# Optimization experiments

Hardware: AMD Instinct MI355X
Metric: run time of the kernel (lower is better)

The kernel has to match this reference:

```python
import jax, jax.numpy as jnp
import numpy as np

N_NODES = 50000
N_EDGES = 800000
IN_FEATS = 256
OUT_FEATS = 128
NEG_SLOPE = 0.2


def setup_inputs() -> dict:
    key = jax.random.key(0)
    k1, k2, k3, k4 = jax.random.split(key, 4)
    feat = jax.random.normal(k1, (N_NODES, IN_FEATS), dtype=jnp.float32)
    limit = float(np.sqrt(6.0 / (IN_FEATS + OUT_FEATS)))  # xavier_uniform
    W = jax.random.uniform(k2, (IN_FEATS, OUT_FEATS), dtype=jnp.float32,
                           minval=-limit, maxval=limit)
    bias = jnp.zeros((OUT_FEATS,), dtype=jnp.float32)
    src = jax.random.randint(k3, (N_EDGES,), 0, N_NODES, dtype=jnp.int64)
    dst = jax.random.randint(k4, (N_EDGES,), 0, N_NODES, dtype=jnp.int64)
    return {"feat": feat, "W": W, "bias": bias, "src": src, "dst": dst}


def reference(feat, W, bias, src, dst):
    N = feat.shape[0]
    ones = jnp.ones(src.shape[0], dtype=feat.dtype)
    # degrees (clamped to 1, as in the torch code)
    out_deg = jnp.maximum(jax.ops.segment_sum(ones, src, num_segments=N), 1.0)
    in_deg = jnp.maximum(jax.ops.segment_sum(ones, dst, num_segments=N), 1.0)
    # norm == 'both': pre-scale by out-degree^-1/2
    h = feat * (out_deg ** -0.5)[:, None]
    # in_feats > out_feats branch: project first
    h = h @ W  # [N, out_feats]
    hs = h[src]          # [E, out_feats] gather
    hd = jnp.tanh(h[dst])  # [E, out_feats] gather
    e = jnp.sum(hs * hd, axis=1)                      # [E]
    e = jnp.where(e > 0, e, NEG_SLOPE * e)            # leaky_relu(0.2)
    # edge_softmax: softmax over edges grouped by destination node
    emax = jax.ops.segment_max(e, dst, num_segments=N)
    emax = jnp.where(jnp.isfinite(emax), emax, 0.0)   # guard empty groups
    ee = jnp.exp(e - emax[dst])
    esum = jax.ops.segment_sum(ee, dst, num_segments=N)
    e_soft = ee / esum[dst]
    # update_all(copy_u, sum): unweighted scatter-sum of src features into dst
    rst = jax.ops.segment_sum(hs, dst, num_segments=N)  # [N, out_feats]
    # norm == 'both': post-scale by in-degree^-1/2, then bias (activation=None)
    rst = rst * (in_deg ** -0.5)[:, None] + bias
    return rst, e_soft
```

## Files before the change

### kernel.cpp

```cpp
#include <hip/hip_runtime.h>
#include <math.h>

#define NNODES 50000
#define NEDGES 800000
#define INFEAT 256
#define OUTF   128
#define NEG_SLOPE 0.2f
#define MAXDEG 64
#define GBM 64
#define GEMM_NB 782

typedef __attribute__((ext_vector_type(8))) short bf16x8;
typedef __attribute__((ext_vector_type(4))) float f32x4;

__device__ __forceinline__ ushort f2bf(float f) {
    unsigned u = __float_as_uint(f);
    unsigned r = (u + 0x7FFFu + ((u >> 16) & 1u)) >> 16;
    return (ushort)r;
}
__device__ __forceinline__ float bflo(unsigned u) { return __uint_as_float(u << 16); }
__device__ __forceinline__ float bfhi(unsigned u) { return __uint_as_float(u & 0xFFFF0000u); }

__global__ void kzero(int* p, int n) {
    int i = blockIdx.x * 256 + threadIdx.x;
    if (i < n) p[i] = 0;
}

__global__ void kwbt(const float* __restrict__ W, ushort* __restrict__ whi,
                     ushort* __restrict__ wlo) {
    int i = blockIdx.x * 256 + threadIdx.x;
    int n = i >> 8, k = i & 255;
    float w = W[(size_t)k * OUTF + n];
    ushort h = f2bf(w);
    float hf = __uint_as_float((unsigned)h << 16);
    whi[i] = h;
    wlo[i] = f2bf(w - hf);
}

__launch_bounds__(256)
__global__ void kfused(const float* __restrict__ feat, const uint4* __restrict__ whi,
                       const uint4* __restrict__ wlo, unsigned* __restrict__ hb,
                       const int* __restrict__ src, const int* __restrict__ dst,
                       int* __restrict__ cnt_out, int* __restrict__ fill,
                       int* __restrict__ ebd, int M, int E) {
    __shared__ char smem_raw[32768];
    int tid = threadIdx.x;

    if (blockIdx.x & 1) {
        for (int i = (blockIdx.x >> 1) * 256 + tid; i < E; i += GEMM_NB * 256) {
            atomicAdd(&cnt_out[src[i]], 1);
            int d = dst[i];
            int p = atomicAdd(&fill[d], 1);
            if (p < MAXDEG) ebd[(d << 6) + p] = i;
        }
        return;
    }

    uint4* Bh = (uint4*)smem_raw;
    uint4* Bo = Bh + 1024;
    int lane = tid & 63, wid = tid >> 6;
    int gb = blockIdx.x >> 1;

    int m0 = gb * GBM + wid * 16;
    int arow = m0 + (lane & 15);
    int ar = arow < M ? arow : M - 1;
    const float* ap = &feat[(size_t)ar * INFEAT + ((lane >> 4) << 3)];

    union { uint4 u; bf16x8 s; } ahi[8], alo[8];
    #pragma unroll
    for (int ks = 0; ks < 8; ks++) {
        float4 a0 = *(const float4*)&ap[ks * 32];
        float4 a1 = *(const float4*)&ap[ks * 32 + 4];
        float av[8] = {a0.x, a0.y, a0.z, a0.w, a1.x, a1.y, a1.z, a1.w};
        unsigned hw[4], lw[4];
        #pragma unroll
        for (int q = 0; q < 4; q++) {
            asm("v_cvt_pk_bf16_f32 %0, %1, %2" : "=v"(hw[q]) : "v"(av[2*q]), "v"(av[2*q+1]));
            float h0 = bflo(hw[q]);
            float h1 = bfhi(hw[q]);
            float l0 = av[2*q] - h0;
            float l1 = av[2*q+1] - h1;
            asm("v_cvt_pk_bf16_f32 %0, %1, %2" : "=v"(lw[q]) : "v"(l0), "v"(l1));
        }
        ahi[ks].u = make_uint4(hw[0], hw[1], hw[2], hw[3]);
        alo[ks].u = make_uint4(lw[0], lw[1], lw[2], lw[3]);
    }

    f32x4 acc[8];
    #pragma unroll
    for (int i = 0; i < 8; i++) acc[i] = (f32x4){0.f, 0.f, 0.f, 0.f};

    #pragma unroll
    for (int h = 0; h < 4; h++) {
        __syncthreads();
        #pragma unroll
        for (int r = 0; r < 4; r++) {
            int g = tid + 256 * r;
            int nl = g >> 5, kc = g & 31;
            int gi = (h * 32 + nl) * 32 + kc;
            int li = (nl << 5) | (kc ^ (nl & 7));
            Bh[li] = whi[gi];
            Bo[li] = wlo[gi];
        }
        __syncthreads();
        #pragma unroll
        for (int ks = 0; ks < 8; ks++) {
            int kcb = (ks << 2) + (lane >> 4);
            #pragma unroll
            for (int nt = 0; nt < 2; nt++) {
                int nl = (nt << 4) | (lane & 15);
                int li = (nl << 5) | (kcb ^ (nl & 7));
                union { uint4 u; bf16x8 s; } bh, bo;
                bh.u = Bh[li];
                bo.u = Bo[li];
                int ai = h * 2 + nt;
                acc[ai] = __builtin_amdgcn_mfma_f32_16x16x32_bf16(ahi[ks].s, bh.s, acc[ai], 0, 0, 0);
                acc[ai] = __builtin_amdgcn_mfma_f32_16x16x32_bf16(alo[ks].s, bh.s, acc[ai], 0, 0, 0);
                acc[ai] = __builtin_amdgcn_mfma_f32_16x16x32_bf16(ahi[ks].s, bo.s, acc[ai], 0, 0, 0);
            }
        }
    }

    #pragma unroll
    for (int ai = 0; ai < 8; ai++) {
        #pragma unroll
        for (int q = 0; q < 4; q++) {
            float v = acc[ai][q];
            float vp = __shfl_xor(v, 1, 64);
            int grow = m0 + ((lane >> 4) << 2) + q;
            if (!(lane & 1) && grow < M) {
                unsigned w;
                asm("v_cvt_pk_bf16_f32 %0, %1, %2" : "=v"(w) : "v"(v), "v"(vp));
                hb[(size_t)grow * 64 + ((ai << 4) | (lane & 15)) / 2] = w;
            }
        }
    }
}

__launch_bounds__(256)
__global__ void kaggregate(const unsigned* __restrict__ hb, const int* __restrict__ src,
                           const int* __restrict__ ebd, const int* __restrict__ fill,
                           const int* __restrict__ cnt_out, const float* __restrict__ bias,
                           float* __restrict__ out_rst, float* __restrict__ out_es,
                           int nnodes) {
    __shared__ float thl[4][128];
    int wid = threadIdx.x >> 6;
    int lane = threadIdx.x & 63;
    int n = blockIdx.x * 4 + wid;
    if (n >= nnodes) return;

    int deg = fill[n];
    if (deg > MAXDEG) deg = MAXDEG;
    const int ROWU = OUTF / 2;

    int g = lane >> 3;
    int t = lane & 7;
    int c = t * 16;

    {
        int co = cnt_out[n];
        float sc_d = rsqrtf((float)(co < 1 ? 1 : co));
        unsigned u = hb[(size_t)n * ROWU + lane];
        thl[wid][2 * lane]     = tanhf(sc_d * bflo(u));
        thl[wid][2 * lane + 1] = tanhf(sc_d * bfhi(u));
    }
    float thf[16];
    #pragma unroll
    for (int q = 0; q < 4; q++) {
        float4 v = *(float4*)&thl[wid][c + q * 4];
        thf[q*4+0] = v.x; thf[q*4+1] = v.y; thf[q*4+2] = v.z; thf[q*4+3] = v.w;
    }

    int eid = 0, s = 0;
    if (lane < deg) { eid = ebd[(n << 6) + lane]; s = src[eid]; }

    float accf[16];
    #pragma unroll
    for (int k = 0; k < 16; k++) accf[k] = 0.f;
    float myv = -INFINITY;

    for (int base = 0; base < deg; base += 8) {
        int m = base + g;
        int sj = __shfl(s, m, 64);
        uint4 r0 = make_uint4(0u, 0u, 0u, 0u), r1 = r0;
        float scs = 0.f;
        if (m < deg) {
            const uint4* rp = (const uint4*)&hb[(size_t)sj * ROWU + t * 8];
            r0 = rp[0]; r1 = rp[1];
            int co = cnt_out[sj];
            scs = rsqrtf((float)(co < 1 ? 1 : co));
        }
        unsigned ua[8] = {r0.x, r0.y, r0.z, r0.w, r1.x, r1.y, r1.z, r1.w};
        float pd = 0.f;
        #pragma unroll
        for (int k = 0; k < 8; k++) {
            float lo = bflo(ua[k]), hi = bfhi(ua[k]);
            accf[2*k]   = fmaf(scs, lo, accf[2*k]);
            accf[2*k+1] = fmaf(scs, hi, accf[2*k+1]);
            pd += lo * thf[2*k] + hi * thf[2*k+1];
        }
        #pragma unroll
        for (int msk = 1; msk < 8; msk <<= 1) pd += __shfl_xor(pd, msk, 64);
        float p = scs * pd;
        float e = p > 0.f ? p : NEG_SLOPE * p;
        if (m < deg && t == (base >> 3)) myv = e;
    }

    if (deg > 0) {
        float mx = myv;
        #pragma unroll
        for (int msk = 1; msk < 64; msk <<= 1) mx = fmaxf(mx, __shfl_xor(mx, msk, 64));
        int m = 8 * t + g;
        float v = (m < deg) ? expf(myv - mx) : 0.f;
        float sum = v;
        #pragma unroll
        for (int msk = 1; msk < 64; msk <<= 1) sum += __shfl_xor(sum, msk, 64);
        float inv = 1.f / sum;
        int eidm = __shfl(eid, m, 64);
        if (m < deg) out_es[eidm] = v * inv;
    }

    #pragma unroll
    for (int msk = 8; msk < 64; msk <<= 1) {
        #pragma unroll
        for (int k = 0; k < 16; k++) accf[k] += __shfl_xor(accf[k], msk, 64);
    }
    if (g == 0) {
        float sc = rsqrtf((float)(deg < 1 ? 1 : deg));
        #pragma unroll
        for (int q = 0; q < 4; q++) {
            float4 b = *(const float4*)&bias[c + q * 4];
            float4 r = make_float4(accf[4*q]   * sc + b.x, accf[4*q+1] * sc + b.y,
                                   accf[4*q+2] * sc + b.z, accf[4*q+3] * sc + b.w);
            *(float4*)&out_rst[(size_t)n * OUTF + c + q * 4] = r;
        }
    }
}

extern "C" void kernel_launch(void* const* d_in, const int* in_sizes, int n_in,
                              void* d_out, int out_size, void* d_ws, size_t ws_size,
                              hipStream_t stream) {
    const float* feat = (const float*)d_in[0];
    const float* W    = (const float*)d_in[1];
    const float* bias = (const float*)d_in[2];
    const int*   src  = (const int*)d_in[3];
    const int*   dst  = (const int*)d_in[4];

    float* out_rst = (float*)d_out;
    float* out_es  = (float*)d_out + (size_t)NNODES * OUTF;

    char* ws = (char*)d_ws;
    size_t o = 0;
    auto alloc = [&](size_t bytes) { void* p = ws + o; o += (bytes + 255) & ~(size_t)255; return p; };
    int*    cnt_out = (int*)alloc(NNODES * 4);
    int*    fill    = (int*)alloc(NNODES * 4);
    int*    ebd     = (int*)alloc((size_t)NNODES * MAXDEG * 4);
    ushort* whi     = (ushort*)alloc((size_t)OUTF * INFEAT * 2);
    ushort* wlo     = (ushort*)alloc((size_t)OUTF * INFEAT * 2);
    ushort* hb      = (ushort*)alloc((size_t)NNODES * OUTF * 2);
    (void)o; (void)ws_size; (void)in_sizes; (void)n_in; (void)out_size;

    const int zints = (int)(2 * (((size_t)NNODES * 4 + 255) & ~(size_t)255) / 4);
    kzero<<<(zints + 255) / 256, 256, 0, stream>>>((int*)d_ws, zints);

    kwbt<<<(OUTF * INFEAT + 255) / 256, 256, 0, stream>>>(W, whi, wlo);

    kfused<<<2 * GEMM_NB, 256, 0, stream>>>(feat, (const uint4*)whi, (const uint4*)wlo,
                                            (unsigned*)hb, src, dst,
                                            cnt_out, fill, ebd, NNODES, NEDGES);

    kaggregate<<<(NNODES + 3) / 4, 256, 0, stream>>>((const unsigned*)hb, src, ebd, fill,
                                                     cnt_out, bias, out_rst, out_es, NNODES);
}
```

Measured before the change: 137.6 us.

## Split CSR bucketing across kernels to overlap with aggregation of first node range

Bucketing by destination is now done in two parts. Nodes below a split point are bucketed in the fused GEMM kernel, and the rest are bucketed in a new mixed kernel whose other blocks already aggregate the first node range. A final kernel then aggregates the remaining nodes. The aim is to shorten the atomic-heavy bucketing that sits alongside the GEMM and to overlap the rest with aggregation work, at the cost of an extra launch and reading dst twice. The zeroing kernel is also replaced with hipMemsetAsync.

Result: slower. 144.1 us (+4.7%).

```diff
diff --git a/kernel.cpp b/kernel.cpp
--- a/kernel.cpp
+++ b/kernel.cpp
@@ -9,6 +9,8 @@
 #define MAXDEG 64
 #define GBM 64
 #define GEMM_NB 782
+#define HSPLIT 20000
+#define AGG1_NB 5000
 
 typedef __attribute__((ext_vector_type(8))) short bf16x8;
 typedef __attribute__((ext_vector_type(4))) float f32x4;
@@ -20,11 +22,6 @@
 }
 __device__ __forceinline__ float bflo(unsigned u) { return __uint_as_float(u << 16); }
 __device__ __forceinline__ float bfhi(unsigned u) { return __uint_as_float(u & 0xFFFF0000u); }
-
-__global__ void kzero(int* p, int n) {
-    int i = blockIdx.x * 256 + threadIdx.x;
-    if (i < n) p[i] = 0;
-}
 
 __global__ void kwbt(const float* __restrict__ W, ushort* __restrict__ whi,
                      ushort* __restrict__ wlo) {
@@ -37,6 +34,104 @@
     wlo[i] = f2bf(w - hf);
 }
 
+__device__ __forceinline__ void agg_node(int n, float* thlw,
+                                         const unsigned* __restrict__ hb,
+                                         const int* __restrict__ src,
+                                         const int* __restrict__ ebd,
+                                         const int* __restrict__ fill,
+                                         const int* __restrict__ cnt_out,
+                                         const float* __restrict__ bias,
+                                         float* __restrict__ out_rst,
+                                         float* __restrict__ out_es) {
+    int lane = threadIdx.x & 63;
+    int deg = fill[n];
+    if (deg > MAXDEG) deg = MAXDEG;
+    const int ROWU = OUTF / 2;
+
+    int g = lane >> 3;
+    int t = lane & 7;
+    int c = t * 16;
+
+    {
+        int co = cnt_out[n];
+        float sc_d = rsqrtf((float)(co < 1 ? 1 : co));
+        unsigned u = hb[(size_t)n * ROWU + lane];
+        thlw[2 * lane]     = tanhf(sc_d * bflo(u));
+        thlw[2 * lane + 1] = tanhf(sc_d * bfhi(u));
+    }
+    float thf[16];
+    #pragma unroll
+    for (int q = 0; q < 4; q++) {
+        float4 v = *(float4*)&thlw[c + q * 4];
+        thf[q*4+0] = v.x; thf[q*4+1] = v.y; thf[q*4+2] = v.z; thf[q*4+3] = v.w;
+    }
+
+    int eid = 0, s = 0;
+    if (lane < deg) { eid = ebd[(n << 6) + lane]; s = src[eid]; }
+
+    float accf[16];
+    #pragma unroll
+    for (int k = 0; k < 16; k++) accf[k] = 0.f;
+    float myv = -INFINITY;
+
+    for (int base = 0; base < deg; base += 8) {
+        int m = base + g;
+        int sj = __shfl(s, m, 64);
+        uint4 r0 = make_uint4(0u, 0u, 0u, 0u), r1 = r0;
+        float scs = 0.f;
+        if (m < deg) {
+            const uint4* rp = (const uint4*)&hb[(size_t)sj * ROWU + t * 8];
+            r0 = rp[0]; r1 = rp[1];
+            int co = cnt_out[sj];
+            scs = rsqrtf((float)(co < 1 ? 1 : co));
+        }
+        unsigned ua[8] = {r0.x, r0.y, r0.z, r0.w, r1.x, r1.y, r1.z, r1.w};
+        float pd = 0.f;
+        #pragma unroll
+        for (int k = 0; k < 8; k++) {
+            float lo = bflo(ua[k]), hi = bfhi(ua[k]);
+            accf[2*k]   = fmaf(scs, lo, accf[2*k]);
+            accf[2*k+1] = fmaf(scs, hi, accf[2*k+1]);
+            pd += lo * thf[2*k] + hi * thf[2*k+1];
+        }
+        #pragma unroll
+        for (int msk = 1; msk < 8; msk <<= 1) pd += __shfl_xor(pd, msk, 64);
+        float p = scs * pd;
+        float e = p > 0.f ? p : NEG_SLOPE * p;
+        if (m < deg && t == (base >> 3)) myv = e;
+    }
+
+    if (deg > 0) {
+        float mx = myv;
+        #pragma unroll
+        for (int msk = 1; msk < 64; msk <<= 1) mx = fmaxf(mx, __shfl_xor(mx, msk, 64));
+        int m = 8 * t + g;
+        float v = (m < deg) ? expf(myv - mx) : 0.f;
+        float sum = v;
+        #pragma unroll
+        for (int msk = 1; msk < 64; msk <<= 1) sum += __shfl_xor(sum, msk, 64);
+        float inv = 1.f / sum;
+        int eidm = __shfl(eid, m, 64);
+        if (m < deg) out_es[eidm] = v * inv;
+    }
+
+    #pragma unroll
+    for (int msk = 8; msk < 64; msk <<= 1) {
+        #pragma unroll
+        for (int k = 0; k < 16; k++) accf[k] += __shfl_xor(accf[k], msk, 64);
+    }
+    if (g == 0) {
+        float sc = rsqrtf((float)(deg < 1 ? 1 : deg));
+        #pragma unroll
+        for (int q = 0; q < 4; q++) {
+            float4 b = *(const float4*)&bias[c + q * 4];
+            float4 r = make_float4(accf[4*q]   * sc + b.x, accf[4*q+1] * sc + b.y,
+                                   accf[4*q+2] * sc + b.z, accf[4*q+3] * sc + b.w);
+            *(float4*)&out_rst[(size_t)n * OUTF + c + q * 4] = r;
+        }
+    }
+}
+
 __launch_bounds__(256)
 __global__ void kfused(const float* __restrict__ feat, const uint4* __restrict__ whi,
                        const uint4* __restrict__ wlo, unsigned* __restrict__ hb,
@@ -50,8 +145,10 @@
         for (int i = (blockIdx.x >> 1) * 256 + tid; i < E; i += GEMM_NB * 256) {
             atomicAdd(&cnt_out[src[i]], 1);
             int d = dst[i];
-            int p = atomicAdd(&fill[d], 1);
-            if (p < MAXDEG) ebd[(d << 6) + p] = i;
+            if (d < HSPLIT) {
+                int p = atomicAdd(&fill[d], 1);
+                if (p < MAXDEG) ebd[(d << 6) + p] = i;
+            }
         }
         return;
     }
@@ -138,103 +235,42 @@
 }
 
 __launch_bounds__(256)
-__global__ void kaggregate(const unsigned* __restrict__ hb, const int* __restrict__ src,
-                           const int* __restrict__ ebd, const int* __restrict__ fill,
-                           const int* __restrict__ cnt_out, const float* __restrict__ bias,
-                           float* __restrict__ out_rst, float* __restrict__ out_es,
-                           int nnodes) {
+__global__ void kmix(const unsigned* __restrict__ hb, const int* __restrict__ src,
+                     const int* __restrict__ dst, int* __restrict__ ebd,
+                     int* __restrict__ fill, const int* __restrict__ cnt_out,
+                     const float* __restrict__ bias, float* __restrict__ out_rst,
+                     float* __restrict__ out_es, int E) {
+    __shared__ float thl[4][128];
+    int tid = threadIdx.x;
+
+    if (blockIdx.x & 1) {
+        for (int i = (blockIdx.x >> 1) * 256 + tid; i < E; i += AGG1_NB * 256) {
+            int d = dst[i];
+            if (d >= HSPLIT) {
+                int p = atomicAdd(&fill[d], 1);
+                if (p < MAXDEG) ebd[(d << 6) + p] = i;
+            }
+        }
+        return;
+    }
+
+    int wid = tid >> 6;
+    int n = (blockIdx.x >> 1) * 4 + wid;
+    if (n >= HSPLIT) return;
+    agg_node(n, &thl[wid][0], hb, src, ebd, fill, cnt_out, bias, out_rst, out_es);
+}
+
+__launch_bounds__(256)
+__global__ void kagg(const unsigned* __restrict__ hb, const int* __restrict__ src,
+                     const int* __restrict__ ebd, const int* __restrict__ fill,
+                     const int* __restrict__ cnt_out, const float* __restrict__ bias,
+                     float* __restrict__ out_rst, float* __restrict__ out_es,
+                     int n0, int n1) {
     __shared__ float thl[4][128];
     int wid = threadIdx.x >> 6;
-    int lane = threadIdx.x & 63;
-    int n = blockIdx.x * 4 + wid;
-    if (n >= nnodes) return;
-
-    int deg = fill[n];
-    if (deg > MAXDEG) deg = MAXDEG;
-    const int ROWU = OUTF / 2;
-
-    int g = lane >> 3;
-    int t = lane & 7;
-    int c = t * 16;
-
-    {
-        int co = cnt_out[n];
-        float sc_d = rsqrtf((float)(co < 1 ? 1 : co));
-        unsigned u = hb[(size_t)n * ROWU + lane];
-        thl[wid][2 * lane]     = tanhf(sc_d * bflo(u));
-        thl[wid][2 * lane + 1] = tanhf(sc_d * bfhi(u));
-    }
-    float thf[16];
-    #pragma unroll
-    for (int q = 0; q < 4; q++) {
-        float4 v = *(float4*)&thl[wid][c + q * 4];
-        thf[q*4+0] = v.x; thf[q*4+1] = v.y; thf[q*4+2] = v.z; thf[q*4+3] = v.w;
-    }
-
-    int eid = 0, s = 0;
-    if (lane < deg) { eid = ebd[(n << 6) + lane]; s = src[eid]; }
-
-    float accf[16];
-    #pragma unroll
-    for (int k = 0; k < 16; k++) accf[k] = 0.f;
-    float myv = -INFINITY;
-
-    for (int base = 0; base < deg; base += 8) {
-        int m = base + g;
-        int sj = __shfl(s, m, 64);
-        uint4 r0 = make_uint4(0u, 0u, 0u, 0u), r1 = r0;
-        float scs = 0.f;
-        if (m < deg) {
-            const uint4* rp = (const uint4*)&hb[(size_t)sj * ROWU + t * 8];
-            r0 = rp[0]; r1 = rp[1];
-            int co = cnt_out[sj];
-            scs = rsqrtf((float)(co < 1 ? 1 : co));
-        }
-        unsigned ua[8] = {r0.x, r0.y, r0.z, r0.w, r1.x, r1.y, r1.z, r1.w};
-        float pd = 0.f;
-        #pragma unroll
-        for (int k = 0; k < 8; k++) {
-            float lo = bflo(ua[k]), hi = bfhi(ua[k]);
-            accf[2*k]   = fmaf(scs, lo, accf[2*k]);
-            accf[2*k+1] = fmaf(scs, hi, accf[2*k+1]);
-            pd += lo * thf[2*k] + hi * thf[2*k+1];
-        }
-        #pragma unroll
-        for (int msk = 1; msk < 8; msk <<= 1) pd += __shfl_xor(pd, msk, 64);
-        float p = scs * pd;
-        float e = p > 0.f ? p : NEG_SLOPE * p;
-        if (m < deg && t == (base >> 3)) myv = e;
-    }
-
-    if (deg > 0) {
-        float mx = myv;
-        #pragma unroll
-        for (int msk = 1; msk < 64; msk <<= 1) mx = fmaxf(mx, __shfl_xor(mx, msk, 64));
-        int m = 8 * t + g;
-        float v = (m < deg) ? expf(myv - mx) : 0.f;
-        float sum = v;
-        #pragma unroll
-        for (int msk = 1; msk < 64; msk <<= 1) sum += __shfl_xor(sum, msk, 64);
-        float inv = 1.f / sum;
-        int eidm = __shfl(eid, m, 64);
-        if (m < deg) out_es[eidm] = v * inv;
-    }
-
-    #pragma unroll
-    for (int msk = 8; msk < 64; msk <<= 1) {
-        #pragma unroll
-        for (int k = 0; k < 16; k++) accf[k] += __shfl_xor(accf[k], msk, 64);
-    }
-    if (g == 0) {
-        float sc = rsqrtf((float)(deg < 1 ? 1 : deg));
-        #pragma unroll
-        for (int q = 0; q < 4; q++) {
-            float4 b = *(const float4*)&bias[c + q * 4];
-            float4 r = make_float4(accf[4*q]   * sc + b.x, accf[4*q+1] * sc + b.y,
-                                   accf[4*q+2] * sc + b.z, accf[4*q+3] * sc + b.w);
-            *(float4*)&out_rst[(size_t)n * OUTF + c + q * 4] = r;
-        }
-    }
+    int n = n0 + blockIdx.x * 4 + wid;
+    if (n >= n1) return;
+    agg_node(n, &thl[wid][0], hb, src, ebd, fill, cnt_out, bias, out_rst, out_es);
 }
 
 extern "C" void kernel_launch(void* const* d_in, const int* in_sizes, int n_in,
@@ -260,8 +296,8 @@
     ushort* hb      = (ushort*)alloc((size_t)NNODES * OUTF * 2);
     (void)o; (void)ws_size; (void)in_sizes; (void)n_in; (void)out_size;
 
-    const int zints = (int)(2 * (((size_t)NNODES * 4 + 255) & ~(size_t)255) / 4);
-    kzero<<<(zints + 255) / 256, 256, 0, stream>>>((int*)d_ws, zints);
+    const size_t zbytes = 2 * (((size_t)NNODES * 4 + 255) & ~(size_t)255);
+    hipMemsetAsync(d_ws, 0, zbytes, stream);
 
     kwbt<<<(OUTF * INFEAT + 255) / 256, 256, 0, stream>>>(W, whi, wlo);
 
@@ -269,6 +305,10 @@
                                             (unsigned*)hb, src, dst,
                                             cnt_out, fill, ebd, NNODES, NEDGES);
 
-    kaggregate<<<(NNODES + 3) / 4, 256, 0, stream>>>((const unsigned*)hb, src, ebd, fill,
-                                                     cnt_out, bias, out_rst, out_es, NNODES);
-}
+    kmix<<<2 * AGG1_NB, 256, 0, stream>>>((const unsigned*)hb, src, dst, ebd, fill,
+                                          cnt_out, bias, out_rst, out_es, NEDGES);
+
+    kagg<<<(NNODES - HSPLIT + 3) / 4, 256, 0, stream>>>((const unsigned*)hb, src, ebd, fill,
+                                                        cnt_out, bias, out_rst, out_es,
+                                                        HSPLIT, NNODES);
+}
```

## Replace global out-degree atomics with per-block packed LDS histograms and reduction

Applied to the files above, without the earlier changes.

Out-degree counting moves from global atomicAdd per edge to 128 dedicated blocks that each build a shared-memory histogram, packing four 8-bit counters per word, then write partial histograms that a new reduction kernel sums into cnt_out. The zeroing kernel is replaced by a memset of only the fill array, and the aggregation body is factored into a device helper. This is meant to cut global atomic traffic and contention on cnt_out, at the cost of an extra kernel launch, about 6.4 MB of partial-histogram writes and reads, and 8-bit per-block counters that could overflow if one block saw more than 255 edges from the same source.

After: 117.8 us. -14.4%, faster.

```diff
diff --git a/kernel.cpp b/kernel.cpp
--- a/kernel.cpp
+++ b/kernel.cpp
@@ -9,6 +9,8 @@
 #define MAXDEG 64
 #define GBM 64
 #define GEMM_NB 782
+#define HB 128
+#define HW 12500
 
 typedef __attribute__((ext_vector_type(8))) short bf16x8;
 typedef __attribute__((ext_vector_type(4))) float f32x4;
@@ -20,11 +22,6 @@
 }
 __device__ __forceinline__ float bflo(unsigned u) { return __uint_as_float(u << 16); }
 __device__ __forceinline__ float bfhi(unsigned u) { return __uint_as_float(u & 0xFFFF0000u); }
-
-__global__ void kzero(int* p, int n) {
-    int i = blockIdx.x * 256 + threadIdx.x;
-    if (i < n) p[i] = 0;
-}
 
 __global__ void kwbt(const float* __restrict__ W, ushort* __restrict__ whi,
                      ushort* __restrict__ wlo) {
@@ -41,14 +38,27 @@
 __global__ void kfused(const float* __restrict__ feat, const uint4* __restrict__ whi,
                        const uint4* __restrict__ wlo, unsigned* __restrict__ hb,
                        const int* __restrict__ src, const int* __restrict__ dst,
-                       int* __restrict__ cnt_out, int* __restrict__ fill,
-                       int* __restrict__ ebd, int M, int E) {
-    __shared__ char smem_raw[32768];
+                       int* __restrict__ fill, int* __restrict__ ebd,
+                       unsigned* __restrict__ hist_part, int M, int E) {
+    __shared__ unsigned sh[HW + 300];
     int tid = threadIdx.x;
 
-    if (blockIdx.x & 1) {
-        for (int i = (blockIdx.x >> 1) * 256 + tid; i < E; i += GEMM_NB * 256) {
-            atomicAdd(&cnt_out[src[i]], 1);
+    if (blockIdx.x < HB) {
+        for (int j = tid; j < HW; j += 256) sh[j] = 0;
+        __syncthreads();
+        for (int i = blockIdx.x * 256 + tid; i < E; i += HB * 256) {
+            int s = src[i];
+            atomicAdd(&sh[s >> 2], 1u << ((s & 3) * 8));
+        }
+        __syncthreads();
+        unsigned* gp = hist_part + (size_t)blockIdx.x * HW;
+        for (int j = tid; j < HW; j += 256) gp[j] = sh[j];
+        return;
+    }
+
+    int b2 = blockIdx.x - HB;
+    if (b2 & 1) {
+        for (int i = (b2 >> 1) * 256 + tid; i < E; i += GEMM_NB * 256) {
             int d = dst[i];
             int p = atomicAdd(&fill[d], 1);
             if (p < MAXDEG) ebd[(d << 6) + p] = i;
@@ -56,10 +66,10 @@
         return;
     }
 
-    uint4* Bh = (uint4*)smem_raw;
+    uint4* Bh = (uint4*)sh;
     uint4* Bo = Bh + 1024;
     int lane = tid & 63, wid = tid >> 6;
-    int gb = blockIdx.x >> 1;
+    int gb = b2 >> 1;
 
     int m0 = gb * GBM + wid * 16;
     int arow = m0 + (lane & 15);
@@ -137,18 +147,32 @@
     }
 }
 
-__launch_bounds__(256)
-__global__ void kaggregate(const unsigned* __restrict__ hb, const int* __restrict__ src,
-                           const int* __restrict__ ebd, const int* __restrict__ fill,
-                           const int* __restrict__ cnt_out, const float* __restrict__ bias,
-                           float* __restrict__ out_rst, float* __restrict__ out_es,
-                           int nnodes) {
-    __shared__ float thl[4][128];
-    int wid = threadIdx.x >> 6;
+__global__ void kred(const unsigned* __restrict__ hist_part, int* __restrict__ cnt_out) {
+    int j = blockIdx.x * 256 + threadIdx.x;
+    if (j >= HW) return;
+    unsigned a01 = 0, a23 = 0;
+    for (int b = 0; b < HB; b++) {
+        unsigned v = hist_part[(size_t)b * HW + j];
+        a01 += v & 0x00FF00FFu;
+        a23 += (v >> 8) & 0x00FF00FFu;
+    }
+    int n = j * 4;
+    cnt_out[n]     = (int)(a01 & 0xFFFFu);
+    cnt_out[n + 1] = (int)(a23 & 0xFFFFu);
+    cnt_out[n + 2] = (int)(a01 >> 16);
+    cnt_out[n + 3] = (int)(a23 >> 16);
+}
+
+__device__ __forceinline__ void agg_node(int n, float* thlw,
+                                         const unsigned* __restrict__ hb,
+                                         const int* __restrict__ src,
+                                         const int* __restrict__ ebd,
+                                         const int* __restrict__ fill,
+                                         const int* __restrict__ cnt_out,
+                                         const float* __restrict__ bias,
+                                         float* __restrict__ out_rst,
+                                         float* __restrict__ out_es) {
     int lane = threadIdx.x & 63;
-    int n = blockIdx.x * 4 + wid;
-    if (n >= nnodes) return;
-
     int deg = fill[n];
     if (deg > MAXDEG) deg = MAXDEG;
     const int ROWU = OUTF / 2;
@@ -161,13 +185,13 @@
         int co = cnt_out[n];
         float sc_d = rsqrtf((float)(co < 1 ? 1 : co));
         unsigned u = hb[(size_t)n * ROWU + lane];
-        thl[wid][2 * lane]     = tanhf(sc_d * bflo(u));
-        thl[wid][2 * lane + 1] = tanhf(sc_d * bfhi(u));
+        thlw[2 * lane]     = tanhf(sc_d * bflo(u));
+        thlw[2 * lane + 1] = tanhf(sc_d * bfhi(u));
     }
     float thf[16];
     #pragma unroll
     for (int q = 0; q < 4; q++) {
-        float4 v = *(float4*)&thl[wid][c + q * 4];
+        float4 v = *(float4*)&thlw[c + q * 4];
         thf[q*4+0] = v.x; thf[q*4+1] = v.y; thf[q*4+2] = v.z; thf[q*4+3] = v.w;
     }
 
@@ -237,6 +261,19 @@
     }
 }
 
+__launch_bounds__(256)
+__global__ void kagg(const unsigned* __restrict__ hb, const int* __restrict__ src,
+                     const int* __restrict__ ebd, const int* __restrict__ fill,
+                     const int* __restrict__ cnt_out, const float* __restrict__ bias,
+                     float* __restrict__ out_rst, float* __restrict__ out_es,
+                     int nnodes) {
+    __shared__ float thl[4][128];
+    int wid = threadIdx.x >> 6;
+    int n = blockIdx.x * 4 + wid;
+    if (n >= nnodes) return;
+    agg_node(n, &thl[wid][0], hb, src, ebd, fill, cnt_out, bias, out_rst, out_es);
+}
+
 extern "C" void kernel_launch(void* const* d_in, const int* in_sizes, int n_in,
                               void* d_out, int out_size, void* d_ws, size_t ws_size,
                               hipStream_t stream) {
@@ -252,23 +289,25 @@
     char* ws = (char*)d_ws;
     size_t o = 0;
     auto alloc = [&](size_t bytes) { void* p = ws + o; o += (bytes + 255) & ~(size_t)255; return p; };
-    int*    cnt_out = (int*)alloc(NNODES * 4);
-    int*    fill    = (int*)alloc(NNODES * 4);
-    int*    ebd     = (int*)alloc((size_t)NNODES * MAXDEG * 4);
-    ushort* whi     = (ushort*)alloc((size_t)OUTF * INFEAT * 2);
-    ushort* wlo     = (ushort*)alloc((size_t)OUTF * INFEAT * 2);
-    ushort* hb      = (ushort*)alloc((size_t)NNODES * OUTF * 2);
+    int*      cnt_out   = (int*)alloc(NNODES * 4);
+    int*      fill      = (int*)alloc(NNODES * 4);
+    int*      ebd       = (int*)alloc((size_t)NNODES * MAXDEG * 4);
+    ushort*   whi       = (ushort*)alloc((size_t)OUTF * INFEAT * 2);
+    ushort*   wlo       = (ushort*)alloc((size_t)OUTF * INFEAT * 2);
+    ushort*   hb        = (ushort*)alloc((size_t)NNODES * OUTF * 2);
+    unsigned* hist_part = (unsigned*)alloc((size_t)HB * HW * 4);
     (void)o; (void)ws_size; (void)in_sizes; (void)n_in; (void)out_size;
 
-    const int zints = (int)(2 * (((size_t)NNODES * 4 + 255) & ~(size_t)255) / 4);
-    kzero<<<(zints + 255) / 256, 256, 0, stream>>>((int*)d_ws, zints);
+    hipMemsetAsync(fill, 0, NNODES * 4, stream);
 
     kwbt<<<(OUTF * INFEAT + 255) / 256, 256, 0, stream>>>(W, whi, wlo);
 
-    kfused<<<2 * GEMM_NB, 256, 0, stream>>>(feat, (const uint4*)whi, (const uint4*)wlo,
-                                            (unsigned*)hb, src, dst,
-                                            cnt_out, fill, ebd, NNODES, NEDGES);
-
-    kaggregate<<<(NNODES + 3) / 4, 256, 0, stream>>>((const unsigned*)hb, src, ebd, fill,
-                                                     cnt_out, bias, out_rst, out_es, NNODES);
-}
+    kfused<<<HB + 2 * GEMM_NB, 256, 0, stream>>>(feat, (const uint4*)whi, (const uint4*)wlo,
+                                                 (unsigned*)hb, src, dst,
+                                                 fill, ebd, hist_part, NNODES, NEDGES);
+
+    kred<<<(HW + 255) / 256, 256, 0, stream>>>(hist_part, cnt_out);
+
+    kagg<<<(NNODES + 3) / 4, 256, 0, stream>>>((const unsigned*)hb, src, ebd, fill,
+                                               cnt_out, bias, out_rst, out_es, NNODES);
+}
```
